# Kernel tuning notes

Measured on AMD Instinct MI355X. Metric: run time of the kernel, lower is better.

Reference implementation:

```python
import jax, jax.numpy as jnp
import numpy as np

B, L, FD, G = 256, 512, 64, 32
H1, H2, DH = 512, 512, 256  # leaf_hidden=[512,512], diffuse_hidden=[256]

def _gelu(x):
    return jax.nn.gelu(x, approximate=False)  # torch nn.GELU default (erf)

def setup_inputs() -> dict:
    key = jax.random.key(0)
    ks = jax.random.split(key, 14)
    def lin(k, fan_in, shape):
        s = 1.0 / np.sqrt(fan_in)
        return jax.random.uniform(k, shape, jnp.float32, -s, s)
    return {
        "Xg": jax.random.normal(ks[0], (B, G), jnp.float32),
        "Xl": jax.random.normal(ks[1], (B, L, FD), jnp.float32),
        "W1": lin(ks[2], FD, (FD, H1)), "b1": lin(ks[3], FD, (H1,)),
        "W2": lin(ks[4], H1, (H1, H2)), "b2": lin(ks[5], H1, (H2,)),
        "wa": lin(ks[6], H2, (H2, 1)), "ba": lin(ks[7], H2, (1,)),
        "wt": lin(ks[8], H2, (H2, 1)), "bt": lin(ks[9], H2, (1,)),
        "Wd1": lin(ks[10], G + H2, (G + H2, DH)), "bd1": lin(ks[11], G + H2, (DH,)),
        "Wd2": lin(ks[12], DH, (DH, 1)), "bd2": lin(ks[13], DH, (1,)),
    }

def reference(Xg, Xl, W1, b1, W2, b2, wa, ba, wt, bt, Wd1, bd1, Wd2, bd2):
    # per-leaf MLP encoder: [B, L, FD] -> [B, L, H2]
    h = _gelu(jnp.einsum("blf,fh->blh", Xl, W1) + b1)
    h = _gelu(jnp.einsum("blh,hk->blk", h, W2) + b2)
    absorb = jax.nn.softplus(jnp.einsum("blh,ho->bl", h, wa) + ba[0])  # [B, L]
    atten = jax.nn.softplus(jnp.einsum("blh,ho->bl", h, wt) + bt[0])   # [B, L]
    # flip bottom->top to top->bottom
    absorb_tb = absorb[:, ::-1]
    atten_tb = atten[:, ::-1]
    # T_i = prod_{j<i} exp(-atten_tb_j) = exp(-exclusive_cumsum(atten_tb))
    excl = jnp.cumsum(atten_tb, axis=1) - atten_tb
    T = jnp.exp(-excl)
    captured = jnp.sum(T * absorb_tb, axis=1, keepdims=True)  # [B, 1]
    pooled = jnp.mean(h, axis=1)  # [B, H2]
    z = jnp.concatenate([Xg, pooled], axis=1)
    d = _gelu(z @ Wd1 + bd1) @ Wd2 + bd2  # [B, 1]
    return captured + d
```

## Files before the change

### kernel.cpp

```cpp
#include <hip/hip_runtime.h>
#include <hip/hip_bf16.h>
#include <math.h>

#define B_SZ   256
#define L_SZ   512
#define FD_SZ  64
#define H1_SZ  512
#define H2_SZ  512
#define G_SZ   32
#define DH_SZ  256
#define M_SZ   (B_SZ * L_SZ)

typedef __bf16 bfx8 __attribute__((ext_vector_type(8)));
typedef __bf16 bfx4 __attribute__((ext_vector_type(4)));
typedef float  f32x4 __attribute__((ext_vector_type(4)));
typedef float  f32x16 __attribute__((ext_vector_type(16)));

__device__ __forceinline__ float gelu_exact(float x) {
  return 0.5f * x * (1.0f + erff(x * 0.70710678118654752440f));
}
__device__ __forceinline__ float gelu_fast(float x) {
  float x2 = x * x;
  float w = x * fmaf(0.102943398f, x2, 2.30220931f);
  float e = __builtin_amdgcn_exp2f(-w);
  return x * __builtin_amdgcn_rcpf(1.0f + e);
}
__device__ __forceinline__ float softplus_f(float x) {
  return (x > 20.0f) ? x : log1pf(expf(x));
}
__device__ __forceinline__ __bf16 f2bf(float f) { return (__bf16)f; }

#define ROR_ADD(x, n)                                                          \
  {                                                                            \
    int _t = __builtin_amdgcn_mov_dpp(__builtin_bit_cast(int, (x)),            \
                                      0x120 + (n), 0xF, 0xF, true);            \
    (x) += __builtin_bit_cast(float, _t);                                      \
  }

#define MFMA16(a, b, c) __builtin_amdgcn_mfma_f32_16x16x32_bf16((a), (b), (c), 0, 0, 0)
#define MFMA32(a, b, c) __builtin_amdgcn_mfma_f32_32x32x16_bf16((a), (b), (c), 0, 0, 0)

__global__ void repack_kernel(const float* __restrict__ W1,
                              const float* __restrict__ W2,
                              __bf16* __restrict__ W1p,
                              __bf16* __restrict__ W2p,
                              float* __restrict__ pooled) {
  int t = blockIdx.x * 256 + threadIdx.x;
  if (t < 32768)
    *reinterpret_cast<float4*>(pooled + (size_t)t * 4) = (float4){0.f, 0.f, 0.f, 0.f};
  if (t < 4096) {
    int lane = t & 63, blk = t >> 6;
    int ks = blk & 1, mb = blk >> 1;
    int col = 16 * mb + (lane & 15);
    int kbase = ks * 32 + (lane >> 4) * 8;
    bfx8 o;
#pragma unroll
    for (int j = 0; j < 8; ++j) o[j] = f2bf(W1[(size_t)(kbase + j) * H1_SZ + col]);
    *reinterpret_cast<bfx8*>(W1p + (size_t)t * 8) = o;
  } else if (t < 4096 + 32768) {
    int t2 = t - 4096;
    int lane = t2 & 63, blk = t2 >> 6;
    int ks = blk & 31, nb = blk >> 5;
    int col = 32 * nb + (lane & 31);
    int kbase = 16 * ks + (lane >> 5) * 8;
    bfx8 o;
#pragma unroll
    for (int j = 0; j < 8; ++j) o[j] = f2bf(W2[(size_t)(kbase + j) * H2_SZ + col]);
    *reinterpret_cast<bfx8*>(W2p + (size_t)t2 * 8) = o;
  }
}

__global__ __launch_bounds__(1024, 8) void fused_kernel(
    const float* __restrict__ Xl,
    const __bf16* __restrict__ W1p, const __bf16* __restrict__ W2p,
    const float* __restrict__ b1, const float* __restrict__ b2,
    const float* __restrict__ wa, const float* __restrict__ ba,
    const float* __restrict__ wt, const float* __restrict__ bt,
    float* __restrict__ absorbW, float* __restrict__ attenW,
    float* __restrict__ pooled) {
  __shared__ __bf16 Xs[64 * 64];
  __shared__ __bf16 H1s[64 * 512];
  __shared__ float sl[16 * 64 * 2];

  const int tid = threadIdx.x;
  const int lane = tid & 63;
  const int w = tid >> 6;
  const int g = lane >> 4;
  const int c = lane & 15;
  const int c32 = lane & 31;
  const int kg = lane >> 5;
  const int R0 = blockIdx.x * 64;
  const int bidx = R0 >> 9;

  {
    int idx = tid;
    int r = idx >> 4;
    int c4 = idx & 15;
    float4 v = *reinterpret_cast<const float4*>(Xl + (size_t)(R0 + r) * FD_SZ + c4 * 4);
    bfx4 bv;
    bv[0] = f2bf(v.x); bv[1] = f2bf(v.y); bv[2] = f2bf(v.z); bv[3] = f2bf(v.w);
    int chunk = c4 >> 1;
    int off = r * 64 + (((chunk ^ (r & 7)) << 3) + (c4 & 1) * 4);
    *reinterpret_cast<bfx4*>(&Xs[off]) = bv;
  }
  __syncthreads();

  f32x4 acc1[2][4];
#pragma unroll
  for (int mi = 0; mi < 2; ++mi)
#pragma unroll
    for (int ni = 0; ni < 4; ++ni) acc1[mi][ni] = (f32x4){0.f, 0.f, 0.f, 0.f};

#pragma unroll
  for (int ks = 0; ks < 2; ++ks) {
    bfx8 a1[2];
#pragma unroll
    for (int mi = 0; mi < 2; ++mi) {
      int mb = 2 * w + mi;
      a1[mi] = *reinterpret_cast<const bfx8*>(W1p + ((size_t)(mb * 2 + ks) * 64 + lane) * 8);
    }
    bfx8 bx[4];
#pragma unroll
    for (int ni = 0; ni < 4; ++ni) {
      int r = 16 * ni + c;
      int chunk = ks * 4 + g;
      bx[ni] = *reinterpret_cast<const bfx8*>(&Xs[r * 64 + ((chunk ^ (r & 7)) << 3)]);
    }
#pragma unroll
    for (int mi = 0; mi < 2; ++mi)
#pragma unroll
      for (int ni = 0; ni < 4; ++ni)
        acc1[mi][ni] = MFMA16(a1[mi], bx[ni], acc1[mi][ni]);
  }

#pragma unroll
  for (int mi = 0; mi < 2; ++mi) {
    int mb = 2 * w + mi;
    float4 bias4 = *reinterpret_cast<const float4*>(b1 + 16 * mb + 4 * g);
#pragma unroll
    for (int ni = 0; ni < 4; ++ni) {
      int r = 16 * ni + c;
      bfx4 pv;
      pv[0] = f2bf(gelu_fast(acc1[mi][ni][0] + bias4.x));
      pv[1] = f2bf(gelu_fast(acc1[mi][ni][1] + bias4.y));
      pv[2] = f2bf(gelu_fast(acc1[mi][ni][2] + bias4.z));
      pv[3] = f2bf(gelu_fast(acc1[mi][ni][3] + bias4.w));
      int kchunk = 2 * mb + (g >> 1);
      int off = r * 512 + ((kchunk ^ (r & 31)) << 3) + (g & 1) * 4;
      *reinterpret_cast<bfx4*>(&H1s[off]) = pv;
    }
  }
  __syncthreads();

  f32x16 acc2[2];
#pragma unroll
  for (int m = 0; m < 2; ++m)
#pragma unroll
    for (int q = 0; q < 16; ++q) acc2[m][q] = 0.0f;

  const __bf16* wpb = W2p + ((size_t)w * 32 * 64 + lane) * 8;
  for (int ks = 0; ks < 32; ++ks) {
    bfx8 a2[2];
#pragma unroll
    for (int m = 0; m < 2; ++m) {
      int r = 32 * m + c32;
      int chunk = 2 * ks + kg;
      a2[m] = *reinterpret_cast<const bfx8*>(&H1s[r * 512 + ((chunk ^ (r & 31)) << 3)]);
    }
    bfx8 bw = *reinterpret_cast<const bfx8*>(wpb + (size_t)ks * 512);
    __builtin_amdgcn_s_setprio(1);
    acc2[0] = MFMA32(a2[0], bw, acc2[0]);
    acc2[1] = MFMA32(a2[1], bw, acc2[1]);
    __builtin_amdgcn_s_setprio(0);
  }

  const int col = 32 * w + c32;
  const float b2v = b2[col];
  const float wav = wa[col];
  const float wtv = wt[col];
  float pool0 = 0.0f;
  const int rbase = 4 * kg;
  const bool hi16 = (lane & 16) != 0;

#pragma unroll
  for (int m = 0; m < 2; ++m) {
#pragma unroll
    for (int q = 0; q < 8; ++q) {
      int rA = 2 * q, rB = 2 * q + 1;
      float vA = gelu_fast(acc2[m][rA] + b2v);
      float vB = gelu_fast(acc2[m][rB] + b2v);
      pool0 += vA + vB;
      float saA = vA * wav, saB = vB * wav;
      float stA = vA * wtv, stB = vB * wtv;
      float zs = hi16 ? saB : saA;
      float ys = hi16 ? saA : saB;
      float zt = hi16 ? stB : stA;
      float yt = hi16 ? stA : stB;
      ys = __shfl_xor(ys, 16, 64);
      yt = __shfl_xor(yt, 16, 64);
      float ss = zs + ys;
      float tt = zt + yt;
      ROR_ADD(ss, 8); ROR_ADD(ss, 4); ROR_ADD(ss, 2); ROR_ADD(ss, 1);
      ROR_ADD(tt, 8); ROR_ADD(tt, 4); ROR_ADD(tt, 2); ROR_ADD(tt, 1);
      if (c32 == 0) {
        int row = 32 * m + (rA & 3) + 8 * (rA >> 2) + rbase;
        *reinterpret_cast<float2*>(&sl[w * 128 + row * 2]) = make_float2(ss, tt);
      } else if (c32 == 16) {
        int row = 32 * m + (rB & 3) + 8 * (rB >> 2) + rbase;
        *reinterpret_cast<float2*>(&sl[w * 128 + row * 2]) = make_float2(ss, tt);
      }
    }
  }
  pool0 += __shfl_xor(pool0, 32, 64);
  if (lane < 32)
    atomicAdd(&pooled[bidx * H2_SZ + 32 * w + c32], pool0);
  __syncthreads();

  if (tid < 64) {
    float sa = 0.0f, st = 0.0f;
#pragma unroll
    for (int w16 = 0; w16 < 16; ++w16) {
      float2 v2 = *reinterpret_cast<float2*>(&sl[w16 * 128 + tid * 2]);
      sa += v2.x; st += v2.y;
    }
    absorbW[R0 + tid] = softplus_f(sa + ba[0]);
    attenW[R0 + tid]  = softplus_f(st + bt[0]);
  }
}

__global__ __launch_bounds__(256) void finalize_kernel(
    const float* __restrict__ Xg,
    const float* __restrict__ absorbW, const float* __restrict__ attenW,
    const float* __restrict__ pooled,
    const float* __restrict__ Wd1, const float* __restrict__ bd1,
    const float* __restrict__ Wd2, const float* __restrict__ bd2,
    float* __restrict__ out) {
  __shared__ float s0[512];
  __shared__ float s1[512];
  __shared__ float sab[512];
  __shared__ float zz[544];
  __shared__ float redc[4];
  __shared__ float redd[4];

  const int b = blockIdx.x;
  const int t = threadIdx.x;
  const int i0 = t, i1 = t + 256;

  float a0 = attenW[b * L_SZ + (L_SZ - 1 - i0)];
  float a1 = attenW[b * L_SZ + (L_SZ - 1 - i1)];
  sab[i0] = absorbW[b * L_SZ + (L_SZ - 1 - i0)];
  sab[i1] = absorbW[b * L_SZ + (L_SZ - 1 - i1)];
  s0[i0] = a0; s0[i1] = a1;
  __syncthreads();

  float* src = s0;
  float* dst = s1;
  for (int off = 1; off < 512; off <<= 1) {
    float v0 = src[i0] + ((i0 >= off) ? src[i0 - off] : 0.0f);
    float v1 = src[i1] + ((i1 >= off) ? src[i1 - off] : 0.0f);
    dst[i0] = v0; dst[i1] = v1;
    __syncthreads();
    float* tmp = src; src = dst; dst = tmp;
  }

  float p = expf(-(src[i0] - a0)) * sab[i0] + expf(-(src[i1] - a1)) * sab[i1];
#pragma unroll
  for (int off = 32; off; off >>= 1) p += __shfl_down(p, off, 64);
  if ((t & 63) == 0) redc[t >> 6] = p;

  if (t < G_SZ) zz[t] = Xg[b * G_SZ + t];
  zz[G_SZ + i0] = pooled[b * H2_SZ + i0] * (1.0f / (float)L_SZ);
  zz[G_SZ + i1] = pooled[b * H2_SZ + i1] * (1.0f / (float)L_SZ);
  __syncthreads();

  float s = bd1[t];
  for (int cc = 0; cc < G_SZ + H2_SZ; ++cc) s = fmaf(zz[cc], Wd1[cc * DH_SZ + t], s);
  float v = gelu_exact(s) * Wd2[t];
#pragma unroll
  for (int off = 32; off; off >>= 1) v += __shfl_down(v, off, 64);
  if ((t & 63) == 0) redd[t >> 6] = v;
  __syncthreads();

  if (t == 0) {
    float captured = redc[0] + redc[1] + redc[2] + redc[3];
    float d = redd[0] + redd[1] + redd[2] + redd[3] + bd2[0];
    out[b] = captured + d;
  }
}

extern "C" void kernel_launch(void* const* d_in, const int* in_sizes, int n_in,
                              void* d_out, int out_size, void* d_ws, size_t ws_size,
                              hipStream_t stream) {
  const float* Xg  = (const float*)d_in[0];
  const float* Xl  = (const float*)d_in[1];
  const float* W1  = (const float*)d_in[2];
  const float* b1  = (const float*)d_in[3];
  const float* W2  = (const float*)d_in[4];
  const float* b2  = (const float*)d_in[5];
  const float* wa  = (const float*)d_in[6];
  const float* ba  = (const float*)d_in[7];
  const float* wt  = (const float*)d_in[8];
  const float* bt  = (const float*)d_in[9];
  const float* Wd1 = (const float*)d_in[10];
  const float* bd1 = (const float*)d_in[11];
  const float* Wd2 = (const float*)d_in[12];
  const float* bd2 = (const float*)d_in[13];

  char* ws = (char*)d_ws;
  __bf16* W1p    = (__bf16*)(ws + 0);
  __bf16* W2p    = (__bf16*)(ws + 65536);
  float* absorbW = (float*)(ws + 589824);
  float* attenW  = (float*)(ws + 1114112);
  float* pooled  = (float*)(ws + 1638400);

  repack_kernel<<<144, 256, 0, stream>>>(W1, W2, W1p, W2p, pooled);
  fused_kernel<<<M_SZ / 64, 1024, 0, stream>>>(Xl, W1p, W2p, b1, b2, wa, ba,
                                               wt, bt, absorbW, attenW, pooled);
  finalize_kernel<<<B_SZ, 256, 0, stream>>>(Xg, absorbW, attenW, pooled,
                                            Wd1, bd1, Wd2, bd2, (float*)d_out);
}
```

Baseline: 140.7 us.

## Compute absorb/atten projections with MFMA over bf16 H2 staged in shared memory

Replaces the per-wave shuffle/DPP reductions for the absorb and atten dot products with a small MFMA GEMM. The second-layer activations are written as bf16 into the reused H1 shared buffer, and four waves multiply them by a repacked weight matrix that holds wa and wt in its first two columns. This removes many cross-lane reduction instructions and the separate float staging array. In exchange it adds an extra barrier, shared-memory writes and reads of the whole H2 tile, and bf16 rounding of the activations before the projection.

```diff
diff --git a/kernel.cpp b/kernel.cpp
--- a/kernel.cpp
+++ b/kernel.cpp
@@ -30,20 +30,16 @@
 }
 __device__ __forceinline__ __bf16 f2bf(float f) { return (__bf16)f; }
 
-#define ROR_ADD(x, n)                                                          \
-  {                                                                            \
-    int _t = __builtin_amdgcn_mov_dpp(__builtin_bit_cast(int, (x)),            \
-                                      0x120 + (n), 0xF, 0xF, true);            \
-    (x) += __builtin_bit_cast(float, _t);                                      \
-  }
-
 #define MFMA16(a, b, c) __builtin_amdgcn_mfma_f32_16x16x32_bf16((a), (b), (c), 0, 0, 0)
 #define MFMA32(a, b, c) __builtin_amdgcn_mfma_f32_32x32x16_bf16((a), (b), (c), 0, 0, 0)
 
 __global__ void repack_kernel(const float* __restrict__ W1,
                               const float* __restrict__ W2,
+                              const float* __restrict__ wa,
+                              const float* __restrict__ wt,
                               __bf16* __restrict__ W1p,
                               __bf16* __restrict__ W2p,
+                              __bf16* __restrict__ W3p,
                               float* __restrict__ pooled) {
   int t = blockIdx.x * 256 + threadIdx.x;
   if (t < 32768)
@@ -67,20 +63,30 @@
 #pragma unroll
     for (int j = 0; j < 8; ++j) o[j] = f2bf(W2[(size_t)(kbase + j) * H2_SZ + col]);
     *reinterpret_cast<bfx8*>(W2p + (size_t)t2 * 8) = o;
+  } else if (t < 4096 + 32768 + 1024) {
+    int t3 = t - (4096 + 32768);
+    int lane = t3 & 63, ks = t3 >> 6;
+    int col = lane & 15;
+    int kbase = 32 * ks + (lane >> 4) * 8;
+    bfx8 o;
+#pragma unroll
+    for (int j = 0; j < 8; ++j)
+      o[j] = (col == 0) ? f2bf(wa[kbase + j])
+           : (col == 1) ? f2bf(wt[kbase + j]) : (__bf16)0.0f;
+    *reinterpret_cast<bfx8*>(W3p + (size_t)t3 * 8) = o;
   }
 }
 
 __global__ __launch_bounds__(1024, 8) void fused_kernel(
     const float* __restrict__ Xl,
     const __bf16* __restrict__ W1p, const __bf16* __restrict__ W2p,
+    const __bf16* __restrict__ W3p,
     const float* __restrict__ b1, const float* __restrict__ b2,
-    const float* __restrict__ wa, const float* __restrict__ ba,
-    const float* __restrict__ wt, const float* __restrict__ bt,
+    const float* __restrict__ ba, const float* __restrict__ bt,
     float* __restrict__ absorbW, float* __restrict__ attenW,
     float* __restrict__ pooled) {
   __shared__ __bf16 Xs[64 * 64];
   __shared__ __bf16 H1s[64 * 512];
-  __shared__ float sl[16 * 64 * 2];
 
   const int tid = threadIdx.x;
   const int lane = tid & 63;
@@ -173,58 +179,47 @@
     acc2[1] = MFMA32(a2[1], bw, acc2[1]);
     __builtin_amdgcn_s_setprio(0);
   }
-
-  const int col = 32 * w + c32;
-  const float b2v = b2[col];
-  const float wav = wa[col];
-  const float wtv = wt[col];
+  __syncthreads();
+
+  __bf16* Vs = H1s;
+  const int colg = 32 * w + c32;
+  const float b2v = b2[colg];
+  const int cchunk = colg >> 3;
+  const int clow = colg & 7;
   float pool0 = 0.0f;
-  const int rbase = 4 * kg;
-  const bool hi16 = (lane & 16) != 0;
-
 #pragma unroll
   for (int m = 0; m < 2; ++m) {
 #pragma unroll
-    for (int q = 0; q < 8; ++q) {
-      int rA = 2 * q, rB = 2 * q + 1;
-      float vA = gelu_fast(acc2[m][rA] + b2v);
-      float vB = gelu_fast(acc2[m][rB] + b2v);
-      pool0 += vA + vB;
-      float saA = vA * wav, saB = vB * wav;
-      float stA = vA * wtv, stB = vB * wtv;
-      float zs = hi16 ? saB : saA;
-      float ys = hi16 ? saA : saB;
-      float zt = hi16 ? stB : stA;
-      float yt = hi16 ? stA : stB;
-      ys = __shfl_xor(ys, 16, 64);
-      yt = __shfl_xor(yt, 16, 64);
-      float ss = zs + ys;
-      float tt = zt + yt;
-      ROR_ADD(ss, 8); ROR_ADD(ss, 4); ROR_ADD(ss, 2); ROR_ADD(ss, 1);
-      ROR_ADD(tt, 8); ROR_ADD(tt, 4); ROR_ADD(tt, 2); ROR_ADD(tt, 1);
-      if (c32 == 0) {
-        int row = 32 * m + (rA & 3) + 8 * (rA >> 2) + rbase;
-        *reinterpret_cast<float2*>(&sl[w * 128 + row * 2]) = make_float2(ss, tt);
-      } else if (c32 == 16) {
-        int row = 32 * m + (rB & 3) + 8 * (rB >> 2) + rbase;
-        *reinterpret_cast<float2*>(&sl[w * 128 + row * 2]) = make_float2(ss, tt);
-      }
+    for (int reg = 0; reg < 16; ++reg) {
+      float v = gelu_fast(acc2[m][reg] + b2v);
+      pool0 += v;
+      int row = 32 * m + (reg & 3) + 8 * (reg >> 2) + 4 * kg;
+      Vs[row * 512 + ((cchunk ^ (row & 31)) << 3) + clow] = f2bf(v);
     }
   }
   pool0 += __shfl_xor(pool0, 32, 64);
   if (lane < 32)
-    atomicAdd(&pooled[bidx * H2_SZ + 32 * w + c32], pool0);
-  __syncthreads();
-
-  if (tid < 64) {
-    float sa = 0.0f, st = 0.0f;
-#pragma unroll
-    for (int w16 = 0; w16 < 16; ++w16) {
-      float2 v2 = *reinterpret_cast<float2*>(&sl[w16 * 128 + tid * 2]);
-      sa += v2.x; st += v2.y;
-    }
-    absorbW[R0 + tid] = softplus_f(sa + ba[0]);
-    attenW[R0 + tid]  = softplus_f(st + bt[0]);
+    atomicAdd(&pooled[bidx * H2_SZ + colg], pool0);
+  __syncthreads();
+
+  if (w < 4) {
+    f32x4 racc = (f32x4){0.f, 0.f, 0.f, 0.f};
+    int r = 16 * w + c;
+    for (int ks = 0; ks < 16; ++ks) {
+      int chunk = 4 * ks + g;
+      bfx8 av = *reinterpret_cast<const bfx8*>(&Vs[r * 512 + ((chunk ^ (r & 31)) << 3)]);
+      bfx8 bw3 = *reinterpret_cast<const bfx8*>(W3p + ((size_t)ks * 64 + lane) * 8);
+      racc = MFMA16(av, bw3, racc);
+    }
+    if (c == 0) {
+#pragma unroll
+      for (int reg = 0; reg < 4; ++reg)
+        absorbW[R0 + 16 * w + 4 * g + reg] = softplus_f(racc[reg] + ba[0]);
+    } else if (c == 1) {
+#pragma unroll
+      for (int reg = 0; reg < 4; ++reg)
+        attenW[R0 + 16 * w + 4 * g + reg] = softplus_f(racc[reg] + bt[0]);
+    }
   }
 }
 
@@ -309,13 +304,14 @@
   char* ws = (char*)d_ws;
   __bf16* W1p    = (__bf16*)(ws + 0);
   __bf16* W2p    = (__bf16*)(ws + 65536);
-  float* absorbW = (float*)(ws + 589824);
-  float* attenW  = (float*)(ws + 1114112);
-  float* pooled  = (float*)(ws + 1638400);
-
-  repack_kernel<<<144, 256, 0, stream>>>(W1, W2, W1p, W2p, pooled);
-  fused_kernel<<<M_SZ / 64, 1024, 0, stream>>>(Xl, W1p, W2p, b1, b2, wa, ba,
-                                               wt, bt, absorbW, attenW, pooled);
+  __bf16* W3p    = (__bf16*)(ws + 589824);
+  float* absorbW = (float*)(ws + 606208);
+  float* attenW  = (float*)(ws + 1130496);
+  float* pooled  = (float*)(ws + 1654784);
+
+  repack_kernel<<<148, 256, 0, stream>>>(W1, W2, wa, wt, W1p, W2p, W3p, pooled);
+  fused_kernel<<<M_SZ / 64, 1024, 0, stream>>>(Xl, W1p, W2p, W3p, b1, b2,
+                                               ba, bt, absorbW, attenW, pooled);
   finalize_kernel<<<B_SZ, 256, 0, stream>>>(Xg, absorbW, attenW, pooled,
                                             Wd1, bd1, Wd2, bd2, (float*)d_out);
 }
```

Result: slower. 146.0 us (+3.8%).
